# Kernel optimization log

Hardware: AMD Instinct MI355X
Metric: run time of the kernel (lower is better)

Reference implementation:

```python
import jax, jax.numpy as jnp
import numpy as np

N_Q_HEADS = 16
N_KV_HEADS = 4
HEAD_DIM = 128
SLIDING_WINDOW = 1024
ROPE_BASE = 1024


def _rope_tables(L, dim):
    # half-truncate RoPE: first dim//4 freqs geometric, next dim//4 zero
    freqs = (1.0 / ROPE_BASE) ** jnp.linspace(0.0, 1.0, num=dim // 4)
    freqs = jnp.concatenate([freqs, jnp.zeros(dim // 4, dtype=freqs.dtype)])
    theta = jnp.arange(L, dtype=jnp.float32)[:, None] * freqs[None, :]  # (L, dim/2)
    cos = jnp.cos(theta)[None, :, None, :]  # (1, L, 1, dim/2)
    sin = jnp.sin(theta)[None, :, None, :]
    return cos, sin


def _rotate(x, cos, sin):
    # x: (B, L, H, D)
    x1, x2 = jnp.split(x, 2, axis=-1)
    return jnp.concatenate([x1 * cos + x2 * sin, -x1 * sin + x2 * cos], axis=-1)


def setup_inputs() -> dict:
    key = jax.random.key(0)
    k1, k2, k3, k4 = jax.random.split(key, 4)
    B, L, D = 1, 2048, 2048
    qkv_dim = (N_Q_HEADS + 2 * N_KV_HEADS) * HEAD_DIM  # 3072
    return {
        "x": jax.random.normal(k1, (B, L, D), dtype=jnp.float32),
        "Wqkv": jax.random.normal(k2, (D, qkv_dim), dtype=jnp.float32) * (D ** -0.5),
        "Wo": jax.random.normal(k3, (N_Q_HEADS * HEAD_DIM, D), dtype=jnp.float32) * ((N_Q_HEADS * HEAD_DIM) ** -0.5),
        "s": jax.random.normal(k4, (1, N_Q_HEADS), dtype=jnp.float32) * 0.1,
    }


def reference(x, Wqkv, Wo, s):
    B, L, D = x.shape
    H, QM, hd = N_KV_HEADS, N_Q_HEADS // N_KV_HEADS, HEAD_DIM

    proj = x @ Wqkv  # (B, L, (Hq + 2*Hkv) * hd)
    q, k, v = jnp.split(proj, (N_Q_HEADS * hd, (N_Q_HEADS + N_KV_HEADS) * hd), axis=-1)

    cos, sin = _rope_tables(L, hd)
    q = _rotate(q.reshape(B, L, -1, hd), cos, sin).reshape(B, L, H, QM, hd)
    k = _rotate(k.reshape(B, L, H, hd), cos, sin)
    v = v.reshape(B, L, H, hd)

    sm_scale = 1.0 / jnp.sqrt(jnp.float32(hd))
    q_pos = jnp.arange(L)[None, :, None]
    k_pos = jnp.arange(L)[None, None, :]
    causal = q_pos >= k_pos                       # (1, L, L)
    window = q_pos < k_pos + SLIDING_WINDOW       # index % 2 == 0 -> window active
    mask = causal & window

    # (B, H, M, Lq, Lk) attention logits
    attn = jnp.einsum("bqhmd,bkhd->bhmqk", q, k) * sm_scale
    # NOTE: faithful to source: -inf placed WHERE mask is True
    attn = jnp.where(mask, -jnp.inf, attn)

    sink = jnp.broadcast_to(s.reshape(B, H, QM, 1, 1), (B, H, QM, L, 1))
    w = jax.nn.softmax(jnp.concatenate([attn, sink], axis=-1), axis=-1)[..., :-1]

    out = jnp.einsum("bhmqk,bkhd->bqhmd", w, v).reshape(B, L, -1)
    return out @ Wo
```

## Files before the change

kernel.cpp:

```cpp
#include <hip/hip_runtime.h>
#include <hip/hip_bf16.h>
#include <math.h>

typedef __bf16 bf16;
typedef __bf16 bf16x8 __attribute__((ext_vector_type(8)));
typedef __bf16 bf16x4v __attribute__((ext_vector_type(4)));
typedef short s16x4 __attribute__((ext_vector_type(4)));
typedef float f32x4 __attribute__((ext_vector_type(4)));

#define GLD16(gp, lp) __builtin_amdgcn_global_load_lds( \
    (__attribute__((address_space(1))) void*)(void*)(gp), \
    (__attribute__((address_space(3))) void*)(lp), 16, 0, 0)

#define L_SEQ 2048
#define D_MODEL 2048
#define QKV_N 3072
#define HD 128
#define QSCALE 0.1275310242959836f
#define LOG2E 1.4426950408889634f

__global__ __launch_bounds__(256) void prep(const float* __restrict__ x,
                                            const float* __restrict__ Wqkv,
                                            const float* __restrict__ Wo,
                                            bf16* __restrict__ xb,
                                            bf16* __restrict__ wqkvT,
                                            bf16* __restrict__ woT) {
    __shared__ float tile[32][33];
    int bid = blockIdx.x;
    if (bid < 4096) {
        int idx = (bid * 256 + threadIdx.x) * 4;
        float4 f = *(const float4*)(x + idx);
        bf16x4v o;
        o.x = (bf16)f.x; o.y = (bf16)f.y; o.z = (bf16)f.z; o.w = (bf16)f.w;
        *(bf16x4v*)(xb + idx) = o;
        return;
    }
    bid -= 4096;
    const float* src; bf16* dst; long ld_s, ld_d; int bx, by;
    if (bid < 6144) { bx = bid % 96; by = bid / 96; src = Wqkv; dst = wqkvT; ld_s = QKV_N; ld_d = D_MODEL; }
    else { bid -= 6144; bx = bid & 63; by = bid >> 6; src = Wo; dst = woT; ld_s = D_MODEL; ld_d = D_MODEL; }
    const int tx = threadIdx.x & 31, ty = threadIdx.x >> 5;
    const long c = bx * 32 + tx, r0 = by * 32;
#pragma unroll
    for (int i = 0; i < 4; ++i)
        tile[ty + i * 8][tx] = src[(r0 + ty + i * 8) * ld_s + c];
    __syncthreads();
    const long c0 = bx * 32;
#pragma unroll
    for (int i = 0; i < 4; ++i)
        dst[(c0 + ty + i * 8) * ld_d + r0 + tx] = (bf16)tile[tx][ty + i * 8];
}

__global__ __launch_bounds__(256, 2) void gemm_qkv(const bf16* __restrict__ A,
                                                   const bf16* __restrict__ Bt,
                                                   bf16* __restrict__ Qb,
                                                   bf16* __restrict__ Kb,
                                                   bf16* __restrict__ Vtb) {
    constexpr int KDIM = D_MODEL;
    __shared__ __align__(16) bf16 As[2][128 * 64];
    __shared__ __align__(16) bf16 Bs[2][128 * 64];
    const int tid = threadIdx.x;
    const int wid = tid >> 6, lane = tid & 63;
    const int quad = lane >> 4, l15 = lane & 15;
    const int wm = wid & 1, wn = wid >> 1;
    const int head = blockIdx.x;
    const long m0 = (long)blockIdx.y * 128, n0 = (long)head * 128;

    f32x4 acc[4][4];
#pragma unroll
    for (int i = 0; i < 4; ++i)
#pragma unroll
        for (int j = 0; j < 4; ++j) acc[i][j] = (f32x4){0.f, 0.f, 0.f, 0.f};

    const int srow8 = lane >> 3;
    const int schunk = lane & 7;

    auto stage = [&](int k0, int buf) {
#pragma unroll
        for (int ii = 0; ii < 4; ++ii) {
            const int rowb = wid * 32 + ii * 8;
            const int row = rowb + srow8;
            const int gcol = (schunk ^ (row & 7)) * 8;
            GLD16(A  + (m0 + row) * KDIM + k0 + gcol, &As[buf][rowb * 64]);
            GLD16(Bt + (n0 + row) * KDIM + k0 + gcol, &Bs[buf][rowb * 64]);
        }
    };
    stage(0, 0);

    for (int k0 = 0; k0 < KDIM; k0 += 64) {
        __syncthreads();
        if (k0 + 64 < KDIM) stage(k0 + 64, ((k0 >> 6) + 1) & 1);
        const int buf = (k0 >> 6) & 1;
#pragma unroll
        for (int ks = 0; ks < 2; ++ks) {
            const int pos = ((ks * 4 + quad) ^ (l15 & 7)) * 8;
            bf16x8 af[4], bfr[4];
#pragma unroll
            for (int i = 0; i < 4; ++i)
                af[i] = *(const bf16x8*)&As[buf][(wm * 64 + i * 16 + l15) * 64 + pos];
#pragma unroll
            for (int j = 0; j < 4; ++j)
                bfr[j] = *(const bf16x8*)&Bs[buf][(j * 32 + wn * 16 + l15) * 64 + pos];
#pragma unroll
            for (int i = 0; i < 4; ++i)
#pragma unroll
                for (int j = 0; j < 4; ++j)
                    acc[i][j] = __builtin_amdgcn_mfma_f32_16x16x32_bf16(af[i], bfr[j], acc[i][j], 0, 0, 0);
        }
    }

    if (head < 20) {
        const float sc = head < 16 ? QSCALE : 1.0f;
        bf16* dst = head < 16 ? Qb + (long)head * L_SEQ * HD
                              : Kb + (long)(head - 16) * L_SEQ * HD;
        const int d0 = wn * 16 + l15;
        const float freq = exp2f((float)d0 * (-10.0f / 31.0f));
        const int d1 = 32 + wn * 16 + l15;
#pragma unroll
        for (int i = 0; i < 4; ++i)
#pragma unroll
            for (int r = 0; r < 4; ++r) {
                const long row = m0 + wm * 64 + i * 16 + quad * 4 + r;
                float sn, cs;
                sincosf((float)row * freq, &sn, &cs);
                const float x1 = acc[i][0][r], x2 = acc[i][2][r];
                bf16* p = dst + row * HD;
                p[d0]      = (bf16)((x1 * cs + x2 * sn) * sc);
                p[d0 + 64] = (bf16)((x2 * cs - x1 * sn) * sc);
                p[d1]      = (bf16)(acc[i][1][r] * sc);
                p[d1 + 64] = (bf16)(acc[i][3][r] * sc);
            }
    } else {
        bf16* dst = Vtb + (long)(head - 20) * HD * L_SEQ;
#pragma unroll
        for (int i = 0; i < 4; ++i) {
            const long m = m0 + wm * 64 + i * 16 + quad * 4;
#pragma unroll
            for (int j = 0; j < 4; ++j) {
                const int d = j * 32 + wn * 16 + l15;
                bf16x4v vv;
#pragma unroll
                for (int r = 0; r < 4; ++r) vv[r] = (bf16)acc[i][j][r];
                *(bf16x4v*)(dst + (long)d * L_SEQ + m) = vv;
            }
        }
    }
}

__global__ __launch_bounds__(256) void gemm_out(const bf16* __restrict__ A,
                                                const bf16* __restrict__ Bt,
                                                float* __restrict__ C) {
    constexpr int KDIM = D_MODEL;
    __shared__ __align__(16) bf16 As[64 * 32];
    __shared__ __align__(16) bf16 Bs[128 * 32];
    const int tid = threadIdx.x;
    const int wid = tid >> 6, lane = tid & 63;
    const int quad = lane >> 4, l15 = lane & 15;
    const long m0 = (long)blockIdx.y * 64, n0 = (long)blockIdx.x * 128;
    const int srowA = wid * 16 + (lane >> 2);
    const int srowB = wid * 32 + (lane >> 2);
    const int scol = ((lane & 3) ^ ((lane >> 3) & 3)) * 8;
    f32x4 acc[8];
#pragma unroll
    for (int j = 0; j < 8; ++j) acc[j] = (f32x4){0.f, 0.f, 0.f, 0.f};
    const bf16* Ap  = A  + (m0 + srowA) * KDIM + scol;
    const bf16* Bp  = Bt + (n0 + srowB) * KDIM + scol;
    const bf16* Bp2 = Bp + (long)16 * KDIM;
    bf16* lA  = &As[(wid * 16) * 32];
    bf16* lB  = &Bs[(wid * 32) * 32];
    bf16* lB2 = &Bs[(wid * 32 + 16) * 32];
    const int rsw = ((l15 >> 1) & 3);
    for (int k0 = 0; k0 < KDIM; k0 += 32) {
        GLD16(Ap + k0, lA);
        GLD16(Bp + k0, lB);
        GLD16(Bp2 + k0, lB2);
        __syncthreads();
        bf16x8 af = *(const bf16x8*)&As[(wid * 16 + l15) * 32 + (quad ^ rsw) * 8];
        bf16x8 bfr[8];
#pragma unroll
        for (int j = 0; j < 8; ++j)
            bfr[j] = *(const bf16x8*)&Bs[(j * 16 + l15) * 32 + (quad ^ rsw) * 8];
#pragma unroll
        for (int j = 0; j < 8; ++j)
            acc[j] = __builtin_amdgcn_mfma_f32_16x16x32_bf16(af, bfr[j], acc[j], 0, 0, 0);
        __syncthreads();
    }
#pragma unroll
    for (int j = 0; j < 8; ++j) {
        const long m = m0 + wid * 16 + quad * 4;
        const long n = n0 + j * 16 + l15;
#pragma unroll
        for (int r = 0; r < 4; ++r)
            C[(m + r) * (long)D_MODEL + n] = acc[j][r];
    }
}

__global__ __launch_bounds__(256, 2) void attn_p(const bf16* __restrict__ Qb,
                                                 const bf16* __restrict__ Kb,
                                                 const bf16* __restrict__ Vtb,
                                                 bf16* __restrict__ Opart,
                                                 float* __restrict__ lpart) {
    __shared__ __align__(1024) char smem[65536];

    const int bid = blockIdx.x;
    int t, hq, half;
    if (bid < 256) { t = bid >> 5; hq = (bid & 31) >> 1; half = bid & 1; }
    else { int b2 = bid - 256; t = 8 + (b2 >> 5); hq = (b2 & 31) >> 1; half = b2 & 1; }
    const int h = hq >> 2;
    const int q0 = t * 128;
    const int tid = threadIdx.x;
    const int w = tid >> 6;
    const int lane = tid & 63;
    const int quad = lane >> 4, l15 = lane & 15;

    const bf16* Qg = Qb + (long)hq * L_SEQ * HD;
    const bf16* Kg = Kb + (long)h * L_SEQ * HD;
    const bf16* Vg = Vtb + (long)h * HD * L_SEQ;

    bf16x8 qb[2][4];
#pragma unroll
    for (int rf = 0; rf < 2; ++rf)
#pragma unroll
        for (int kkd = 0; kkd < 4; ++kkd)
            qb[rf][kkd] = *(const bf16x8*)(Qg + (long)(q0 + w * 32 + rf * 16 + l15) * HD
                                              + kkd * 32 + quad * 8);

    f32x4 oaccT[2][8];
#pragma unroll
    for (int rf = 0; rf < 2; ++rf)
#pragma unroll
        for (int j = 0; j < 8; ++j) oaccT[rf][j] = (f32x4){0.f, 0.f, 0.f, 0.f};
    float lacc[2] = {0.f, 0.f};

    const int locnt = (2 * t - 14 > 0) ? (2 * t - 14) : 0;
    const int n = locnt + 32 - 2 * t;
    const int cnt = n >> 1;

    auto ktile = [&](int idx) {
        const int i = 2 * idx + half;
        return (i < locnt) ? i : (2 * t + (i - locnt));
    };

    auto stage = [&](int idx, int buf) {
        const int k0 = ktile(idx) * 64;
        bf16* Ksb  = (bf16*)(smem + buf * 32768);
        bf16* Vtsb = (bf16*)(smem + buf * 32768 + 16384);
#pragma unroll
        for (int ii = 0; ii < 4; ++ii) {
            int rowb = w * 16 + ii * 4;
            int row = rowb + quad;
            GLD16(Kg + (long)(k0 + row) * HD + ((l15 ^ (row & 7)) * 8), &Ksb[rowb * 128]);
        }
#pragma unroll
        for (int ii = 0; ii < 4; ++ii) {
            int rowb = w * 32 + ii * 8;
            int row = rowb + (lane >> 3);
            GLD16(Vg + (long)row * L_SEQ + k0 + (((lane & 7) ^ (row & 7)) * 8), &Vtsb[rowb * 64]);
        }
    };

    stage(0, 0);

    for (int it = 0; it < cnt; ++it) {
        __syncthreads();
        if (it + 1 < cnt) stage(it + 1, (it + 1) & 1);

        const int kt = ktile(it);
        const int k0 = kt * 64;
        const bf16* Ks  = (const bf16*)(smem + (it & 1) * 32768);
        const bf16* Vts = (const bf16*)(smem + (it & 1) * 32768 + 16384);

        f32x4 sacc[2][4];
#pragma unroll
        for (int kb = 0; kb < 4; ++kb) {
            bf16x8 ka[4];
#pragma unroll
            for (int kkd = 0; kkd < 4; ++kkd)
                ka[kkd] = *(const bf16x8*)&Ks[(kb * 16 + l15) * 128 +
                                              (((kkd * 4 + quad) ^ (l15 & 7)) * 8)];
#pragma unroll
            for (int rf = 0; rf < 2; ++rf) {
                f32x4 acc = (f32x4){0.f, 0.f, 0.f, 0.f};
#pragma unroll
                for (int kkd = 0; kkd < 4; ++kkd)
                    acc = __builtin_amdgcn_mfma_f32_16x16x32_bf16(ka[kkd], qb[rf][kkd], acc, 0, 0, 0);
                sacc[rf][kb] = acc;
            }
        }

        const bool bnd = (kt == 2 * t) || (kt == 2 * t + 1) ||
                         (kt == 2 * t - 15) || (kt == 2 * t - 16);
        s16x4 pb[2][4];
#pragma unroll
        for (int rf = 0; rf < 2; ++rf) {
            const int qq = q0 + w * 32 + rf * 16 + l15;
#pragma unroll
            for (int kb = 0; kb < 4; ++kb) {
#pragma unroll
                for (int r = 0; r < 4; ++r) {
                    float v = sacc[rf][kb][r];
                    if (bnd) {
                        const int kk = k0 + kb * 16 + quad * 4 + r;
                        if (!((kk > qq) || (kk <= qq - 1024))) v = -1e30f;
                    }
                    const float p = exp2f(v);
                    lacc[rf] += p;
                    bf16 hp = (bf16)p;
                    pb[rf][kb][r] = __builtin_bit_cast(short, hp);
                }
            }
        }

#pragma unroll
        for (int j = 0; j < 8; ++j) {
            const int drow = j * 16 + l15;
#pragma unroll
            for (int kq = 0; kq < 4; ++kq) {
                const int pc = ((kq * 2 + (quad >> 1)) ^ (l15 & 7));
                s16x4 va = *(const s16x4*)((const char*)&Vts[drow * 64] + pc * 16 + (quad & 1) * 8);
#pragma unroll
                for (int rf = 0; rf < 2; ++rf)
                    oaccT[rf][j] = __builtin_amdgcn_mfma_f32_16x16x16bf16_1k(
                        va, pb[rf][kq], oaccT[rf][j], 0, 0, 0);
            }
        }
    }

#pragma unroll
    for (int rf = 0; rf < 2; ++rf) {
        lacc[rf] += __shfl_xor(lacc[rf], 16, 64);
        lacc[rf] += __shfl_xor(lacc[rf], 32, 64);
    }

    bf16* Od = Opart + (long)bid * 16384;
#pragma unroll
    for (int rf = 0; rf < 2; ++rf) {
        const int ql = w * 32 + rf * 16 + l15;
#pragma unroll
        for (int j = 0; j < 8; ++j) {
            bf16x4v ov;
#pragma unroll
            for (int r = 0; r < 4; ++r) ov[r] = (bf16)oaccT[rf][j][r];
            *(bf16x4v*)(Od + ql * 128 + j * 16 + quad * 4) = ov;
        }
        if (quad == 0) lpart[bid * 128 + ql] = lacc[rf];
    }
}

__global__ __launch_bounds__(256) void attn_combine(const bf16* __restrict__ Opart,
                                                    const float* __restrict__ lpart,
                                                    const float* __restrict__ sink,
                                                    bf16* __restrict__ attnb) {
    const int job = blockIdx.x >> 3, sub = blockIdx.x & 7;
    const int t = job >> 4, hq = job & 15;
    const int bid0 = (t < 8) ? (t * 32 + hq * 2) : (256 + (t - 8) * 32 + hq * 2);
    const int bid1 = bid0 + 1;
    const int e = sub * 2048 + threadIdx.x * 8;
    const int q = e >> 7, d0 = e & 127;
    bf16x8 o0 = *(const bf16x8*)(Opart + (long)bid0 * 16384 + q * 128 + d0);
    bf16x8 o1 = *(const bf16x8*)(Opart + (long)bid1 * 16384 + q * 128 + d0);
    const float l = lpart[bid0 * 128 + q] + lpart[bid1 * 128 + q] +
                    exp2f(sink[hq] * LOG2E);
    const float inv = 1.0f / l;
    bf16x8 ov;
#pragma unroll
    for (int r = 0; r < 8; ++r)
        ov[r] = (bf16)(((float)o0[r] + (float)o1[r]) * inv);
    *(bf16x8*)(attnb + (long)(t * 128 + q) * D_MODEL + hq * 128 + d0) = ov;
}

extern "C" void kernel_launch(void* const* d_in, const int* in_sizes, int n_in,
                              void* d_out, int out_size, void* d_ws, size_t ws_size,
                              hipStream_t stream) {
    (void)in_sizes; (void)n_in; (void)out_size; (void)ws_size;
    const float* x    = (const float*)d_in[0];
    const float* Wqkv = (const float*)d_in[1];
    const float* Wo   = (const float*)d_in[2];
    const float* s    = (const float*)d_in[3];
    float* out = (float*)d_out;

    char* ws = (char*)d_ws;
    bf16* xb    = (bf16*)ws;
    bf16* wqkvT = (bf16*)(ws + 8388608);
    bf16* Qb    = (bf16*)(ws + 20971520);
    bf16* Kb    = (bf16*)(ws + 29360128);
    bf16* Vtb   = (bf16*)(ws + 31457280);
    bf16* woT   = (bf16*)(ws + 33554432);
    bf16* attnb = (bf16*)(ws + 41943040);
    bf16* Opart = (bf16*)ws;
    float* lpart = (float*)(ws + 16777216);

    prep<<<14336, 256, 0, stream>>>(x, Wqkv, Wo, xb, wqkvT, woT);

    gemm_qkv<<<dim3(QKV_N / 128, L_SEQ / 128), 256, 0, stream>>>(
        xb, wqkvT, Qb, Kb, Vtb);

    attn_p<<<512, 256, 0, stream>>>(Qb, Kb, Vtb, Opart, lpart);

    attn_combine<<<2048, 256, 0, stream>>>(Opart, lpart, s, attnb);

    gemm_out<<<dim3(D_MODEL / 128, L_SEQ / 64), 256, 0, stream>>>(
        attnb, woT, out);
}
```

Measured before the change: 218.7 us.

## Shrink QKV GEMM tile to 64 rows and double-buffer output GEMM

The QKV projection GEMM now uses 64x128 tiles instead of 128x128. That doubles the grid to 768 blocks, better filling the 256 CUs, and the smaller LDS footprint allows three blocks per CU. The output GEMM is rewritten to use the same double-buffered 64-wide K staging with a 2x2 wave layout, replacing its single-buffered K=32 loop that synchronised twice per step. The cost is less operand reuse per block and more global traffic for the B matrix.

```diff
diff --git a/kernel.cpp b/kernel.cpp
--- a/kernel.cpp
+++ b/kernel.cpp
@@ -51,24 +51,24 @@
         dst[(c0 + ty + i * 8) * ld_d + r0 + tx] = (bf16)tile[tx][ty + i * 8];
 }
 
-__global__ __launch_bounds__(256, 2) void gemm_qkv(const bf16* __restrict__ A,
+__global__ __launch_bounds__(256, 3) void gemm_qkv(const bf16* __restrict__ A,
                                                    const bf16* __restrict__ Bt,
                                                    bf16* __restrict__ Qb,
                                                    bf16* __restrict__ Kb,
                                                    bf16* __restrict__ Vtb) {
     constexpr int KDIM = D_MODEL;
-    __shared__ __align__(16) bf16 As[2][128 * 64];
+    __shared__ __align__(16) bf16 As[2][64 * 64];
     __shared__ __align__(16) bf16 Bs[2][128 * 64];
     const int tid = threadIdx.x;
     const int wid = tid >> 6, lane = tid & 63;
     const int quad = lane >> 4, l15 = lane & 15;
     const int wm = wid & 1, wn = wid >> 1;
     const int head = blockIdx.x;
-    const long m0 = (long)blockIdx.y * 128, n0 = (long)head * 128;
-
-    f32x4 acc[4][4];
-#pragma unroll
-    for (int i = 0; i < 4; ++i)
+    const long m0 = (long)blockIdx.y * 64, n0 = (long)head * 128;
+
+    f32x4 acc[2][4];
+#pragma unroll
+    for (int i = 0; i < 2; ++i)
 #pragma unroll
         for (int j = 0; j < 4; ++j) acc[i][j] = (f32x4){0.f, 0.f, 0.f, 0.f};
 
@@ -76,12 +76,18 @@
     const int schunk = lane & 7;
 
     auto stage = [&](int k0, int buf) {
+#pragma unroll
+        for (int ii = 0; ii < 2; ++ii) {
+            const int rowb = wid * 16 + ii * 8;
+            const int row = rowb + srow8;
+            const int gcol = (schunk ^ (row & 7)) * 8;
+            GLD16(A + (m0 + row) * KDIM + k0 + gcol, &As[buf][rowb * 64]);
+        }
 #pragma unroll
         for (int ii = 0; ii < 4; ++ii) {
             const int rowb = wid * 32 + ii * 8;
             const int row = rowb + srow8;
             const int gcol = (schunk ^ (row & 7)) * 8;
-            GLD16(A  + (m0 + row) * KDIM + k0 + gcol, &As[buf][rowb * 64]);
             GLD16(Bt + (n0 + row) * KDIM + k0 + gcol, &Bs[buf][rowb * 64]);
         }
     };
@@ -94,15 +100,15 @@
 #pragma unroll
         for (int ks = 0; ks < 2; ++ks) {
             const int pos = ((ks * 4 + quad) ^ (l15 & 7)) * 8;
-            bf16x8 af[4], bfr[4];
-#pragma unroll
-            for (int i = 0; i < 4; ++i)
-                af[i] = *(const bf16x8*)&As[buf][(wm * 64 + i * 16 + l15) * 64 + pos];
+            bf16x8 af[2], bfr[4];
+#pragma unroll
+            for (int i = 0; i < 2; ++i)
+                af[i] = *(const bf16x8*)&As[buf][(wm * 32 + i * 16 + l15) * 64 + pos];
 #pragma unroll
             for (int j = 0; j < 4; ++j)
                 bfr[j] = *(const bf16x8*)&Bs[buf][(j * 32 + wn * 16 + l15) * 64 + pos];
 #pragma unroll
-            for (int i = 0; i < 4; ++i)
+            for (int i = 0; i < 2; ++i)
 #pragma unroll
                 for (int j = 0; j < 4; ++j)
                     acc[i][j] = __builtin_amdgcn_mfma_f32_16x16x32_bf16(af[i], bfr[j], acc[i][j], 0, 0, 0);
@@ -117,10 +123,10 @@
         const float freq = exp2f((float)d0 * (-10.0f / 31.0f));
         const int d1 = 32 + wn * 16 + l15;
 #pragma unroll
-        for (int i = 0; i < 4; ++i)
+        for (int i = 0; i < 2; ++i)
 #pragma unroll
             for (int r = 0; r < 4; ++r) {
-                const long row = m0 + wm * 64 + i * 16 + quad * 4 + r;
+                const long row = m0 + wm * 32 + i * 16 + quad * 4 + r;
                 float sn, cs;
                 sincosf((float)row * freq, &sn, &cs);
                 const float x1 = acc[i][0][r], x2 = acc[i][2][r];
@@ -133,8 +139,8 @@
     } else {
         bf16* dst = Vtb + (long)(head - 20) * HD * L_SEQ;
 #pragma unroll
-        for (int i = 0; i < 4; ++i) {
-            const long m = m0 + wm * 64 + i * 16 + quad * 4;
+        for (int i = 0; i < 2; ++i) {
+            const long m = m0 + wm * 32 + i * 16 + quad * 4;
 #pragma unroll
             for (int j = 0; j < 4; ++j) {
                 const int d = j * 32 + wn * 16 + l15;
@@ -147,52 +153,77 @@
     }
 }
 
-__global__ __launch_bounds__(256) void gemm_out(const bf16* __restrict__ A,
-                                                const bf16* __restrict__ Bt,
-                                                float* __restrict__ C) {
+__global__ __launch_bounds__(256, 3) void gemm_out(const bf16* __restrict__ A,
+                                                   const bf16* __restrict__ Bt,
+                                                   float* __restrict__ C) {
     constexpr int KDIM = D_MODEL;
-    __shared__ __align__(16) bf16 As[64 * 32];
-    __shared__ __align__(16) bf16 Bs[128 * 32];
+    __shared__ __align__(16) bf16 As[2][64 * 64];
+    __shared__ __align__(16) bf16 Bs[2][128 * 64];
     const int tid = threadIdx.x;
     const int wid = tid >> 6, lane = tid & 63;
     const int quad = lane >> 4, l15 = lane & 15;
+    const int wm = wid & 1, wn = wid >> 1;
     const long m0 = (long)blockIdx.y * 64, n0 = (long)blockIdx.x * 128;
-    const int srowA = wid * 16 + (lane >> 2);
-    const int srowB = wid * 32 + (lane >> 2);
-    const int scol = ((lane & 3) ^ ((lane >> 3) & 3)) * 8;
-    f32x4 acc[8];
-#pragma unroll
-    for (int j = 0; j < 8; ++j) acc[j] = (f32x4){0.f, 0.f, 0.f, 0.f};
-    const bf16* Ap  = A  + (m0 + srowA) * KDIM + scol;
-    const bf16* Bp  = Bt + (n0 + srowB) * KDIM + scol;
-    const bf16* Bp2 = Bp + (long)16 * KDIM;
-    bf16* lA  = &As[(wid * 16) * 32];
-    bf16* lB  = &Bs[(wid * 32) * 32];
-    bf16* lB2 = &Bs[(wid * 32 + 16) * 32];
-    const int rsw = ((l15 >> 1) & 3);
-    for (int k0 = 0; k0 < KDIM; k0 += 32) {
-        GLD16(Ap + k0, lA);
-        GLD16(Bp + k0, lB);
-        GLD16(Bp2 + k0, lB2);
+
+    f32x4 acc[2][4];
+#pragma unroll
+    for (int i = 0; i < 2; ++i)
+#pragma unroll
+        for (int j = 0; j < 4; ++j) acc[i][j] = (f32x4){0.f, 0.f, 0.f, 0.f};
+
+    const int srow8 = lane >> 3;
+    const int schunk = lane & 7;
+
+    auto stage = [&](int k0, int buf) {
+#pragma unroll
+        for (int ii = 0; ii < 2; ++ii) {
+            const int rowb = wid * 16 + ii * 8;
+            const int row = rowb + srow8;
+            const int gcol = (schunk ^ (row & 7)) * 8;
+            GLD16(A + (m0 + row) * KDIM + k0 + gcol, &As[buf][rowb * 64]);
+        }
+#pragma unroll
+        for (int ii = 0; ii < 4; ++ii) {
+            const int rowb = wid * 32 + ii * 8;
+            const int row = rowb + srow8;
+            const int gcol = (schunk ^ (row & 7)) * 8;
+            GLD16(Bt + (n0 + row) * KDIM + k0 + gcol, &Bs[buf][rowb * 64]);
+        }
+    };
+    stage(0, 0);
+
+    for (int k0 = 0; k0 < KDIM; k0 += 64) {
         __syncthreads();
-        bf16x8 af = *(const bf16x8*)&As[(wid * 16 + l15) * 32 + (quad ^ rsw) * 8];
-        bf16x8 bfr[8];
-#pragma unroll
-        for (int j = 0; j < 8; ++j)
-            bfr[j] = *(const bf16x8*)&Bs[(j * 16 + l15) * 32 + (quad ^ rsw) * 8];
-#pragma unroll
-        for (int j = 0; j < 8; ++j)
-            acc[j] = __builtin_amdgcn_mfma_f32_16x16x32_bf16(af, bfr[j], acc[j], 0, 0, 0);
-        __syncthreads();
-    }
-#pragma unroll
-    for (int j = 0; j < 8; ++j) {
-        const long m = m0 + wid * 16 + quad * 4;
-        const long n = n0 + j * 16 + l15;
-#pragma unroll
-        for (int r = 0; r < 4; ++r)
-            C[(m + r) * (long)D_MODEL + n] = acc[j][r];
-    }
+        if (k0 + 64 < KDIM) stage(k0 + 64, ((k0 >> 6) + 1) & 1);
+        const int buf = (k0 >> 6) & 1;
+#pragma unroll
+        for (int ks = 0; ks < 2; ++ks) {
+            const int pos = ((ks * 4 + quad) ^ (l15 & 7)) * 8;
+            bf16x8 af[2], bfr[4];
+#pragma unroll
+            for (int i = 0; i < 2; ++i)
+                af[i] = *(const bf16x8*)&As[buf][(wm * 32 + i * 16 + l15) * 64 + pos];
+#pragma unroll
+            for (int j = 0; j < 4; ++j)
+                bfr[j] = *(const bf16x8*)&Bs[buf][(j * 32 + wn * 16 + l15) * 64 + pos];
+#pragma unroll
+            for (int i = 0; i < 2; ++i)
+#pragma unroll
+                for (int j = 0; j < 4; ++j)
+                    acc[i][j] = __builtin_amdgcn_mfma_f32_16x16x32_bf16(af[i], bfr[j], acc[i][j], 0, 0, 0);
+        }
+    }
+
+#pragma unroll
+    for (int i = 0; i < 2; ++i)
+#pragma unroll
+        for (int j = 0; j < 4; ++j) {
+            const long row = m0 + wm * 32 + i * 16 + quad * 4;
+            const long col = n0 + j * 32 + wn * 16 + l15;
+#pragma unroll
+            for (int r = 0; r < 4; ++r)
+                C[(row + r) * (long)D_MODEL + col] = acc[i][j][r];
+        }
 }
 
 __global__ __launch_bounds__(256, 2) void attn_p(const bf16* __restrict__ Qb,
@@ -392,7 +423,7 @@
 
     prep<<<14336, 256, 0, stream>>>(x, Wqkv, Wo, xb, wqkvT, woT);
 
-    gemm_qkv<<<dim3(QKV_N / 128, L_SEQ / 128), 256, 0, stream>>>(
+    gemm_qkv<<<dim3(QKV_N / 128, L_SEQ / 64), 256, 0, stream>>>(
         xb, wqkvT, Qb, Kb, Vtb);
 
     attn_p<<<512, 256, 0, stream>>>(Qb, Kb, Vtb, Opart, lpart);
```

Result: no change. 218.4 us (-0.1%).
